# Optimization experiments

Hardware: AMD Instinct MI355X
Metric: run time of the kernel (lower is better)

## Reference

```python
import jax, jax.numpy as jnp
import numpy as np
from jax import lax


def grid_sample(img, grid):
    """Bilinear grid_sample, align_corners=True, zeros padding.
    img: [N, C, H, W]; grid: [N, Hg, Wg, 2] with (x, y) in [-1, 1].
    Returns [N, C, Hg, Wg]."""
    N, C, H, W = img.shape
    Hg, Wg = grid.shape[1], grid.shape[2]
    gx = (grid[..., 0] + 1.0) * 0.5 * (W - 1)
    gy = (grid[..., 1] + 1.0) * 0.5 * (H - 1)
    x0 = jnp.floor(gx); y0 = jnp.floor(gy)
    x1 = x0 + 1.0;      y1 = y0 + 1.0
    wx1 = gx - x0; wx0 = 1.0 - wx1
    wy1 = gy - y0; wy0 = 1.0 - wy1
    flat = img.reshape(N, C, H * W)

    def corner(ix, iy, w):
        valid = (ix >= 0) & (ix <= W - 1) & (iy >= 0) & (iy <= H - 1)
        ixc = jnp.clip(ix, 0, W - 1).astype(jnp.int32)
        iyc = jnp.clip(iy, 0, H - 1).astype(jnp.int32)
        idx = (iyc * W + ixc).reshape(N, -1)                      # [N, Hg*Wg]
        vals = jnp.take_along_axis(flat, idx[:, None, :], axis=2)  # [N, C, Hg*Wg]
        return vals * (w * valid).reshape(N, 1, -1)

    out = (corner(x0, y0, wx0 * wy0) + corner(x1, y0, wx1 * wy0)
           + corner(x0, y1, wx0 * wy1) + corner(x1, y1, wx1 * wy1))
    return out.reshape(N, C, Hg, Wg)


def ref_points(H, W, dtype=jnp.float32):
    # normalized reference points in (y, x) order, align with torch linspace(0.5, H-0.5, H)
    ry = ((jnp.arange(H, dtype=dtype) + 0.5) / H) * 2.0 - 1.0
    rx = ((jnp.arange(W, dtype=dtype) + 0.5) / W) * 2.0 - 1.0
    gy, gx = jnp.meshgrid(ry, rx, indexing='ij')
    return jnp.stack([gy, gx], axis=-1)  # [H, W, 2]


def conv1x1(x, w, b=None):
    # x: [B, Cin, H, W], w: [Cout, Cin]
    y = jnp.einsum('bchw,oc->bohw', x, w)
    if b is not None:
        y = y + b[None, :, None, None]
    return y


def setup_inputs() -> dict:
    key = jax.random.key(0)
    ks = jax.random.split(key, 16)
    B, nc, H, W = 4, 512, 32, 32
    heads, hc = 8, 64
    gc = 512  # n_group_channels (n_groups = 1)
    s = lambda fan: 1.0 / np.sqrt(fan)
    inp = {
        'x': jax.random.normal(ks[0], (B, nc, H, W), jnp.float32),
        'dw_w': jax.random.normal(ks[1], (gc, 1, 3, 3), jnp.float32) * s(9),
        'dw_b': jnp.zeros((gc,), jnp.float32),
        'ln_w': jnp.ones((gc,), jnp.float32),
        'ln_b': jnp.zeros((gc,), jnp.float32),
        'pw_w': jax.random.normal(ks[2], (2, gc), jnp.float32) * s(gc),
        'q_w': jax.random.normal(ks[3], (nc, nc), jnp.float32) * s(nc),
        'q_b': jnp.zeros((nc,), jnp.float32),
        'k_w': jax.random.normal(ks[4], (nc, nc), jnp.float32) * s(nc),
        'k_b': jnp.zeros((nc,), jnp.float32),
        'v_w': jax.random.normal(ks[5], (nc, nc), jnp.float32) * s(nc),
        'v_b': jnp.zeros((nc,), jnp.float32),
        'rpe_table': jax.random.normal(ks[6], (heads, 2 * H - 1, 2 * W - 1), jnp.float32) * 0.01,
        'gamma': jnp.full((1,), 0.1, jnp.float32),
    }
    return inp


def reference(x, dw_w, dw_b, ln_w, ln_b, pw_w, q_w, q_b, k_w, k_b, v_w, v_b, rpe_table, gamma):
    B, C, H, W = x.shape
    heads, hc = 8, 64
    g = 1
    gc = C // g
    gh = heads // g
    scale = hc ** (-0.5)
    offset_range_factor = 2.0

    # q projection (1x1 conv)
    q = conv1x1(x, q_w, q_b)                                       # [B, C, H, W]

    # offset network: depthwise 3x3 conv -> channel LayerNorm -> GELU -> 1x1 conv to 2ch
    q_off = q.reshape(B * g, gc, H, W)
    h = lax.conv_general_dilated(q_off, dw_w, (1, 1), 'SAME',
                                 dimension_numbers=('NCHW', 'OIHW', 'NCHW'),
                                 feature_group_count=gc)
    h = h + dw_b[None, :, None, None]
    mu = jnp.mean(h, axis=1, keepdims=True)
    var = jnp.mean(jnp.square(h - mu), axis=1, keepdims=True)
    h = (h - mu) * lax.rsqrt(var + 1e-5)
    h = h * ln_w[None, :, None, None] + ln_b[None, :, None, None]
    h = jax.nn.gelu(h, approximate=False)
    offset = jnp.einsum('bchw,oc->bohw', h, pw_w)                  # [B*g, 2, Hk, Wk]
    Hk, Wk = offset.shape[2], offset.shape[3]
    n = Hk * Wk
    rng = jnp.array([1.0 / Hk, 1.0 / Wk], x.dtype).reshape(1, 2, 1, 1)
    offset = jnp.tanh(offset) * rng * offset_range_factor
    offset = jnp.transpose(offset, (0, 2, 3, 1))                   # [B*g, Hk, Wk, 2] (y, x)

    reference_pts = ref_points(Hk, Wk, x.dtype)                    # [Hk, Wk, 2]
    pos = offset + reference_pts[None]                             # [B*g, Hk, Wk, 2]

    # deformable feature sampling
    x_sampled = grid_sample(x.reshape(B * g, gc, H, W), pos[..., ::-1])
    x_sampled = x_sampled.reshape(B, C, n)                         # [B, C, n]

    k = jnp.einsum('oc,bcn->bon', k_w, x_sampled) + k_b[None, :, None]
    v = jnp.einsum('oc,bcn->bon', v_w, x_sampled) + v_b[None, :, None]

    qf = q.reshape(B, heads, hc, H * W)
    kf = k.reshape(B, heads, hc, n)
    vf = v.reshape(B, heads, hc, n)

    attn = jnp.einsum('bhcm,bhcn->bhmn', qf, kf) * scale           # [B, heads, HW, n]

    # relative position bias via grid_sample over rpe table
    rpe = jnp.broadcast_to(rpe_table[None], (B, heads, 2 * H - 1, 2 * W - 1))
    rpe = rpe.reshape(B * g, gh, 2 * H - 1, 2 * W - 1)
    q_grid = ref_points(H, W, x.dtype).reshape(H * W, 2)           # [HW, 2]
    disp = (q_grid[None, :, None, :] - pos.reshape(B * g, n, 2)[:, None, :, :]) * 0.5
    bias = grid_sample(rpe, disp[..., ::-1])                       # [B*g, gh, HW, n]
    attn = attn + bias.reshape(B, heads, H * W, n)

    attn = jax.nn.softmax(attn, axis=-1)
    out = jnp.einsum('bhmn,bhcn->bhcm', attn, vf).reshape(B, C, H, W)
    out = gamma.reshape(()) * out + x
    return out, attn.reshape(B * heads, H * W, n)
```

## Files before the change

kernel.cpp:

```cpp
#include <hip/hip_runtime.h>
#include <hip/hip_bf16.h>
#include <math.h>

typedef short bf16x8 __attribute__((ext_vector_type(8)));
typedef _Float16 f16x8 __attribute__((ext_vector_type(8)));
typedef float f32x4 __attribute__((ext_vector_type(4)));
typedef _Float16 h2 __attribute__((ext_vector_type(2)));

__device__ inline short f2bf(float f) {
    union { float f; unsigned u; } v; v.f = f;
    unsigned r = v.u + 0x7FFFu + ((v.u >> 16) & 1u);
    return (short)(r >> 16);
}
__device__ inline float bf2f(short s) {
    union { unsigned u; float f; } v; v.u = ((unsigned)(unsigned short)s) << 16;
    return v.f;
}
__device__ inline h2 pkrtz(float a, float b) {
    return __builtin_bit_cast(h2, __builtin_amdgcn_cvt_pkrtz(a, b));
}
__device__ inline float fast_exp2(float x) {
    float r;
    asm("v_exp_f32 %0, %1" : "=v"(r) : "v"(x));
    return r;
}
__device__ inline float dot2(h2 a, h2 b) {
#if __has_builtin(__builtin_amdgcn_fdot2)
    return __builtin_amdgcn_fdot2(a, b, 0.f, false);
#else
    return (float)a[0] * (float)b[0] + (float)a[1] * (float)b[1];
#endif
}
__device__ inline void nt_store4(float4 v, float* p) {
    __builtin_nontemporal_store(__builtin_bit_cast(f32x4, v), (f32x4*)p);
}

__global__ __launch_bounds__(256) void prep_x(
    const float* __restrict__ x, short* __restrict__ xt,
    const float* __restrict__ qw, const float* __restrict__ kw,
    const float* __restrict__ vw, short* __restrict__ qwb,
    short* __restrict__ kwb, short* __restrict__ vwb,
    const float* __restrict__ rpe, unsigned* __restrict__ rpet)
{
    __shared__ float ts[64][65];
    int t = threadIdx.x;
    if (blockIdx.z == 5) {
        if (blockIdx.y != 0 || blockIdx.x >= 8) return;
        int hh = blockIdx.x;
        const float* rh = rpe + hh * 3969;
        const float L2E = 1.44269504f;
        #pragma unroll
        for (int i = 0; i < 17; ++i) {
            int j = i * 256 + t;
            if (j < 4225) {
                int iy = j / 65;
                int ix = j - iy * 65;
                float v0 = 0.f, v1 = 0.f;
                if (iy >= 1 && iy <= 63) {
                    const float* rr = rh + (iy - 1) * 63;
                    if (ix >= 1 && ix <= 63) v0 = rr[ix - 1] * L2E;
                    if (ix <= 62)            v1 = rr[ix] * L2E;
                }
                h2 pr; pr[0] = (_Float16)v0; pr[1] = (_Float16)v1;
                rpet[hh * 4225 + j] = __builtin_bit_cast(unsigned, pr);
            }
        }
        return;
    }
    if (blockIdx.z == 4) {
        int f = blockIdx.y * 16 + blockIdx.x;
        int base = (f * 256 + t) * 8;
        #pragma unroll
        for (int w = 0; w < 3; ++w) {
            const float* src = (w == 0) ? qw : (w == 1) ? kw : vw;
            short* dst = (w == 0) ? qwb : (w == 1) ? kwb : vwb;
            float4 f0 = *(const float4*)(src + base);
            float4 f1 = *(const float4*)(src + base + 4);
            bf16x8 o;
            o[0] = f2bf(f0.x); o[1] = f2bf(f0.y); o[2] = f2bf(f0.z); o[3] = f2bf(f0.w);
            o[4] = f2bf(f1.x); o[5] = f2bf(f1.y); o[6] = f2bf(f1.z); o[7] = f2bf(f1.w);
            *(bf16x8*)(dst + base) = o;
        }
        return;
    }
    int p0 = blockIdx.x * 64, c0 = blockIdx.y * 64, b = blockIdx.z;
    #pragma unroll
    for (int i = 0; i < 16; ++i) {
        int idx = i * 256 + t;
        int cl = idx >> 6, pl = idx & 63;
        ts[cl][pl] = x[((size_t)(b * 512 + c0 + cl)) * 1024 + p0 + pl];
    }
    __syncthreads();
    #pragma unroll
    for (int i = 0; i < 16; ++i) {
        int idx = i * 256 + t;
        int pl = idx >> 6, cl = idx & 63;
        xt[((size_t)(b * 1024 + p0 + pl)) * 512 + c0 + cl] = f2bf(ts[cl][pl]);
    }
}

__device__ inline void nt_tile_64x128(const short* __restrict__ A,
                                      const short* __restrict__ B,
                                      int m0, int n0, int t,
                                      short (*As)[32], short (*Bs)[32],
                                      f32x4 (&acc)[2][4])
{
    int wid = t >> 6, l = t & 63;
    int wm = wid >> 1, wn = wid & 1;
    int srB = t >> 1, halfB = t & 1;
    int swB = (srB >> 1) & 3;
    int sB0 = (halfB * 2) ^ swB, sB1 = (halfB * 2 + 1) ^ swB;
    int srA = t >> 2, qA = t & 3;
    int sA = qA ^ ((srA >> 1) & 3);
    for (int k0 = 0; k0 < 512; k0 += 32) {
        const int4 a0 = *(const int4*)(A + (size_t)(m0 + srA) * 512 + k0 + qA * 8);
        const int4 b0 = *(const int4*)(B + (size_t)(n0 + srB) * 512 + k0 + halfB * 16);
        const int4 b1 = *(const int4*)(B + (size_t)(n0 + srB) * 512 + k0 + halfB * 16 + 8);
        __syncthreads();
        *(int4*)&As[srA][sA * 8] = a0;
        *(int4*)&Bs[srB][sB0 * 8] = b0;
        *(int4*)&Bs[srB][sB1 * 8] = b1;
        __syncthreads();
        bf16x8 af[2], bfr[4];
        #pragma unroll
        for (int mt = 0; mt < 2; ++mt) {
            int r = wm * 32 + mt * 16 + (l & 15);
            af[mt] = *(const bf16x8*)&As[r][(((l >> 4)) ^ ((r >> 1) & 3)) * 8];
        }
        #pragma unroll
        for (int nt = 0; nt < 4; ++nt) {
            int r = wn * 64 + nt * 16 + (l & 15);
            bfr[nt] = *(const bf16x8*)&Bs[r][(((l >> 4)) ^ ((r >> 1) & 3)) * 8];
        }
        #pragma unroll
        for (int mt = 0; mt < 2; ++mt)
            #pragma unroll
            for (int nt = 0; nt < 4; ++nt)
                acc[mt][nt] = __builtin_amdgcn_mfma_f32_16x16x32_bf16(
                    af[mt], bfr[nt], acc[mt][nt], 0, 0, 0);
    }
}

__global__ __launch_bounds__(256) void gemm_q(
    const short* __restrict__ A, const short* __restrict__ B,
    const float* __restrict__ bias, short* __restrict__ Ob)
{
    __shared__ short As[64][32];
    __shared__ short Bs[128][32];
    int m0 = blockIdx.x * 64, n0 = blockIdx.y * 128;
    int t = threadIdx.x, wid = t >> 6, l = t & 63;
    int wm = wid >> 1, wn = wid & 1;
    f32x4 acc[2][4] = {};
    nt_tile_64x128(A, B, m0, n0, t, As, Bs, acc);
    #pragma unroll
    for (int mt = 0; mt < 2; ++mt)
        #pragma unroll
        for (int nt = 0; nt < 4; ++nt)
            #pragma unroll
            for (int r = 0; r < 4; ++r) {
                int m = m0 + wm * 32 + mt * 16 + (l >> 4) * 4 + r;
                int n = n0 + wn * 64 + nt * 16 + (l & 15);
                Ob[(size_t)m * 512 + n] = f2bf(acc[mt][nt][r] + bias[n]);
            }
}

__global__ __launch_bounds__(256) void gemm_kv(
    const short* __restrict__ xsb, const short* __restrict__ kwb,
    const float* __restrict__ k_b, short* __restrict__ kfr,
    const short* __restrict__ vwb, const float* __restrict__ v_b,
    short* __restrict__ vfr)
{
    __shared__ short As[64][32];
    __shared__ short Bs[128][32];
    int bid = blockIdx.x;
    int t = threadIdx.x, wid = t >> 6, l = t & 63;
    int wm = wid >> 1, wn = wid & 1;
    f32x4 acc[2][4] = {};
    if (bid < 256) {
        int m0 = (bid >> 5) * 64, n0 = (bid & 31) * 128;
        nt_tile_64x128(kwb, xsb, m0, n0, t, As, Bs, acc);
        int h = m0 >> 6;
        #pragma unroll
        for (int mt = 0; mt < 2; ++mt) {
            int ch0 = m0 + wm * 32 + mt * 16 + (l >> 4) * 4;
            float4 kb4 = *(const float4*)(k_b + ch0);
            int frag = (ch0 >> 5) & 1, gg = (ch0 >> 3) & 3, e = ch0 & 7;
            #pragma unroll
            for (int nt = 0; nt < 4; ++nt) {
                int sm = n0 + wn * 64 + nt * 16 + (l & 15);
                int bq = sm >> 10, p = sm & 1023;
                int T = p >> 4, cs = p & 15;
                uint2 w;
                w.x = (unsigned)(unsigned short)f2bf(acc[mt][nt][0] + kb4.x)
                    | ((unsigned)(unsigned short)f2bf(acc[mt][nt][1] + kb4.y) << 16);
                w.y = (unsigned)(unsigned short)f2bf(acc[mt][nt][2] + kb4.z)
                    | ((unsigned)(unsigned short)f2bf(acc[mt][nt][3] + kb4.w) << 16);
                *(uint2*)(kfr + ((((size_t)(bq * 8 + h) * 64 + T) * 2 + frag) * 64
                                 + gg * 16 + cs) * 8 + e) = w;
            }
        }
    } else {
        int id2 = bid - 256;
        int z = id2 >> 6, rr2 = id2 & 63;
        int m0 = (rr2 >> 2) * 64, n0 = (rr2 & 3) * 128;
        nt_tile_64x128(xsb + (size_t)z * 524288, vwb, m0, n0, t, As, Bs, acc);
        #pragma unroll
        for (int mt = 0; mt < 2; ++mt) {
            int p0 = m0 + wm * 32 + mt * 16 + (l >> 4) * 4;
            int cc = p0 >> 5, gg = (p0 >> 3) & 3, e = p0 & 7;
            #pragma unroll
            for (int nt = 0; nt < 4; ++nt) {
                int ch = n0 + wn * 64 + nt * 16 + (l & 15);
                int h = ch >> 6, wg = (ch & 63) >> 4, cs = ch & 15;
                float vb = v_b[ch];
                h2 plo, phi;
                plo[0] = (_Float16)(acc[mt][nt][0] + vb);
                plo[1] = (_Float16)(acc[mt][nt][1] + vb);
                phi[0] = (_Float16)(acc[mt][nt][2] + vb);
                phi[1] = (_Float16)(acc[mt][nt][3] + vb);
                uint2 w;
                w.x = __builtin_bit_cast(unsigned, plo);
                w.y = __builtin_bit_cast(unsigned, phi);
                *(uint2*)(vfr + ((((size_t)(z * 8 + h) * 4 + wg) * 32 + cc) * 64
                                 + gg * 16 + cs) * 8 + e) = w;
            }
        }
    }
}

__global__ __launch_bounds__(256) void offset_sample(
    const short* __restrict__ qbf, const float* __restrict__ dw_w,
    const float* __restrict__ dw_b, const float* __restrict__ ln_w,
    const float* __restrict__ ln_b, const float* __restrict__ pw_w,
    const short* __restrict__ xt, float* __restrict__ pos,
    short* __restrict__ xs)
{
    __shared__ float red[8];
    __shared__ float2 psh;
    int bid = blockIdx.x;
    int b = bid >> 10, p = bid & 1023;
    int y = p >> 5, x = p & 31;
    int t = threadIdx.x;
    int c0 = 2 * t;
    const short* qb = qbf + (size_t)b * 524288;
    float h0, h1;
    {
        const float* w0 = dw_w + c0 * 9;
        const float* w1 = w0 + 9;
        float s0 = 0.f, s1 = 0.f;
        #pragma unroll
        for (int ky = 0; ky < 3; ++ky) {
            int yy = y + ky - 1;
            if (yy < 0 || yy > 31) continue;
            #pragma unroll
            for (int kx = 0; kx < 3; ++kx) {
                int xx = x + kx - 1;
                if (xx < 0 || xx > 31) continue;
                unsigned u = *(const unsigned*)(qb + (size_t)(yy * 32 + xx) * 512 + c0);
                s0 += bf2f((short)(u & 0xFFFF)) * w0[ky * 3 + kx];
                s1 += bf2f((short)(u >> 16)) * w1[ky * 3 + kx];
            }
        }
        float2 db = *(const float2*)(dw_b + c0);
        h0 = s0 + db.x; h1 = s1 + db.y;
    }
    float ls = h0 + h1;
    float lq = h0 * h0 + h1 * h1;
    #pragma unroll
    for (int s = 32; s >= 1; s >>= 1) {
        ls += __shfl_xor(ls, s);
        lq += __shfl_xor(lq, s);
    }
    int wid = t >> 6, lane = t & 63;
    if (lane == 0) { red[wid] = ls; red[4 + wid] = lq; }
    __syncthreads();
    float mu  = (red[0] + red[1] + red[2] + red[3]) * (1.f / 512.f);
    float var = (red[4] + red[5] + red[6] + red[7]) * (1.f / 512.f) - mu * mu;
    float rstd = rsqrtf(var + 1e-5f);
    float o0, o1;
    {
        float2 lw = *(const float2*)(ln_w + c0);
        float2 lb = *(const float2*)(ln_b + c0);
        float2 p0 = *(const float2*)(pw_w + c0);
        float2 p1 = *(const float2*)(pw_w + 512 + c0);
        float hn0 = (h0 - mu) * rstd * lw.x + lb.x;
        float hn1 = (h1 - mu) * rstd * lw.y + lb.y;
        float g0 = 0.5f * hn0 * (1.f + erff(hn0 * 0.70710678118f));
        float g1 = 0.5f * hn1 * (1.f + erff(hn1 * 0.70710678118f));
        o0 = g0 * p0.x + g1 * p0.y;
        o1 = g0 * p1.x + g1 * p1.y;
    }
    #pragma unroll
    for (int s = 32; s >= 1; s >>= 1) {
        o0 += __shfl_xor(o0, s);
        o1 += __shfl_xor(o1, s);
    }
    __syncthreads();
    if (lane == 0) { red[wid] = o0; red[4 + wid] = o1; }
    __syncthreads();
    if (t == 0) {
        float oy = tanhf(red[0] + red[1] + red[2] + red[3]) * 0.0625f;
        float ox = tanhf(red[4] + red[5] + red[6] + red[7]) * 0.0625f;
        float ry = ((y + 0.5f) * (1.f / 32.f)) * 2.f - 1.f;
        float rx = ((x + 0.5f) * (1.f / 32.f)) * 2.f - 1.f;
        float py = oy + ry, px = ox + rx;
        pos[bid * 2]     = py;
        pos[bid * 2 + 1] = px;
        psh = make_float2(py, px);
    }
    __syncthreads();
    float py = psh.x, px = psh.y;
    float gx = (px + 1.f) * 15.5f;
    float gy = (py + 1.f) * 15.5f;
    float x0f = floorf(gx), y0f = floorf(gy);
    int ix0 = (int)x0f, iy0 = (int)y0f;
    float wx1 = gx - x0f, wx0 = 1.f - wx1;
    float wy1 = gy - y0f, wy0 = 1.f - wy1;
    const short* base = xt + (size_t)b * 524288;
    float a0 = 0.f, a1 = 0.f;
    #pragma unroll
    for (int tap = 0; tap < 4; ++tap) {
        int ix = ix0 + (tap & 1), iy = iy0 + (tap >> 1);
        float w = ((tap & 1) ? wx1 : wx0) * ((tap >> 1) ? wy1 : wy0);
        if (ix >= 0 && ix < 32 && iy >= 0 && iy < 32) {
            unsigned u = *(const unsigned*)(base + (size_t)(iy * 32 + ix) * 512 + c0);
            a0 += bf2f((short)(u & 0xFFFF)) * w;
            a1 += bf2f((short)(u >> 16)) * w;
        }
    }
    unsigned o = ((unsigned)(unsigned short)f2bf(a0)) |
                 (((unsigned)(unsigned short)f2bf(a1)) << 16);
    *(unsigned*)(xs + (size_t)bid * 512 + c0) = o;
}

__global__ __launch_bounds__(512, 4) void attn_fused(
    const short* __restrict__ qbf, const short* __restrict__ kfr,
    const short* __restrict__ vfr, const float* __restrict__ pos,
    const unsigned* __restrict__ rpet, const float* __restrict__ x,
    const float* __restrict__ gamma, float* __restrict__ attn_out,
    float* __restrict__ out0)
{
    __shared__ __align__(16) char smem_raw[33024];
    __shared__ float S_part[16][8];
    h2*     rpe_s = (h2*)smem_raw;
    float2* ccs   = (float2*)(smem_raw + 16960);
    short*  Pn    = (short*)smem_raw;

    int bid = blockIdx.x;
    int xcd = bid & 7, seq = bid >> 3;
    int m0 = (seq & 63) * 16;
    int bh = xcd + 8 * (seq >> 6);
    int b = bh >> 3, h = bh & 7;
    int t = threadIdx.x, wn = t >> 6, l = t & 63;
    int g = l >> 4, c16 = l & 15;

    const unsigned* rt = rpet + h * 4225;
    #pragma unroll
    for (int i = 0; i < 9; ++i) {
        int e = i * 512 + t;
        if (e < 4225) ((unsigned*)rpe_s)[e] = rt[e];
    }
    #pragma unroll
    for (int i = 0; i < 2; ++i) {
        int idx = i * 512 + t;
        float2 pf = *(const float2*)(pos + b * 2048 + idx * 2);
        ccs[idx] = make_float2(fmaf(-15.5f, pf.x, 32.f), fmaf(-15.5f, pf.y, 32.f));
    }
    int rowm = m0 + c16;
    const short* qrow = qbf + ((size_t)(b * 1024 + rowm) * 512 + h * 64 + g * 8);
    bf16x8 aq0 = *(const bf16x8*)qrow;
    bf16x8 aq1 = *(const bf16x8*)(qrow + 32);
    float qy = (((rowm >> 5) + 0.5f) * (1.f / 16.f) - 1.f) * 15.5f;
    float qx = (((rowm & 31) + 0.5f) * (1.f / 16.f) - 1.f) * 15.5f;
    __syncthreads();

    float Ssum = 0.f;
    float e0, e1;
    unsigned ep[16];
    const short* kr = kfr + (size_t)(bh * 64 + wn * 8) * 1024 + l * 8;
    bf16x8 ka0 = *(const bf16x8*)kr;
    bf16x8 kb0 = *(const bf16x8*)(kr + 512);
    bf16x8 ka1 = *(const bf16x8*)(kr + 1024);
    bf16x8 kb1 = *(const bf16x8*)(kr + 1536);
    #pragma unroll
    for (int nt = 0; nt < 8; ++nt) {
        bf16x8 bk0 = ka0, bk1 = kb0;
        ka0 = ka1; kb0 = kb1;
        if (nt < 6) {
            ka1 = *(const bf16x8*)(kr + (nt + 2) * 1024);
            kb1 = *(const bf16x8*)(kr + (nt + 2) * 1024 + 512);
        }
        __builtin_amdgcn_s_setprio(1);
        f32x4 acc = {0.f, 0.f, 0.f, 0.f};
        acc = __builtin_amdgcn_mfma_f32_16x16x32_bf16(bk0, aq0, acc, 0, 0, 0);
        acc = __builtin_amdgcn_mfma_f32_16x16x32_bf16(bk1, aq1, acc, 0, 0, 0);
        __builtin_amdgcn_s_setprio(0);
        int nb = wn * 128 + nt * 16;
        #pragma unroll
        for (int r = 0; r < 4; ++r) {
            float2 cc = ccs[nb + g * 4 + r];
            float gyp = qy + cc.x;
            float gxp = qx + cc.y;
            float fy = floorf(gyp), fx = floorf(gxp);
            float wy1 = gyp - fy, wx1 = gxp - fx;
            int ad = (int)(fy * 65.f + fx);
            h2 r0 = rpe_s[ad];
            h2 r1 = rpe_s[ad + 65];
            h2 wp = pkrtz(1.f - wx1, wx1);
            float t0 = dot2(r0, wp);
            float t1 = dot2(r1, wp);
            float bias2 = t0 + wy1 * (t1 - t0);
            float logit2 = fmaf(acc[r], 0.1803368801f, bias2);
            float e = fast_exp2(logit2);
            Ssum += e;
            if (r == 0) e0 = e;
            else if (r == 1) ep[nt * 2] = __builtin_bit_cast(unsigned, pkrtz(e0, e));
            else if (r == 2) e1 = e;
            else ep[nt * 2 + 1] = __builtin_bit_cast(unsigned, pkrtz(e1, e));
        }
    }
    Ssum += __shfl_xor(Ssum, 16);
    Ssum += __shfl_xor(Ssum, 32);
    if (l < 16) S_part[c16][wn] = Ssum;
    __syncthreads();
    float4 sa = *(const float4*)&S_part[c16][0];
    float4 sb = *(const float4*)&S_part[c16][4];
    float invS = 1.f / (sa.x + sa.y + sa.z + sa.w + sb.x + sb.y + sb.z + sb.w);

    short* prow = Pn + c16 * 1032 + wn * 128;
    #pragma unroll
    for (int nt = 0; nt < 8; ++nt) {
        uint2 w;
        w.x = ep[nt * 2];
        w.y = ep[nt * 2 + 1];
        *(uint2*)(prow + nt * 16 + g * 4) = w;
    }
    __syncthreads();

    size_t obase = ((size_t)(bh * 1024 + m0)) * 1024;
    if (wn >= 4) {
        int tw = t - 256;
        #pragma unroll
        for (int row = 0; row < 16; ++row) {
            float ivr = __shfl(invS, row);
            const unsigned* pr = (const unsigned*)(Pn + row * 1032 + tw * 4);
            unsigned u0 = pr[0], u1 = pr[1];
            h2 a = __builtin_bit_cast(h2, u0);
            h2 bb = __builtin_bit_cast(h2, u1);
            float4 vv = make_float4((float)a[0] * ivr, (float)a[1] * ivr,
                                    (float)bb[0] * ivr, (float)bb[1] * ivr);
            nt_store4(vv, attn_out + obase + (size_t)row * 1024 + tw * 4);
        }
    } else {
        const short* Vb = vfr + (size_t)((bh * 4 + wn) * 32) * 512;
        const short* Prow = Pn + c16 * 1032 + g * 8;
        f32x4 dacc = {0.f, 0.f, 0.f, 0.f};
        __builtin_amdgcn_s_setprio(1);
        #pragma unroll
        for (int cc = 0; cc < 32; ++cc) {
            f16x8 pa  = *(const f16x8*)(Prow + cc * 32);
            f16x8 vb8 = *(const f16x8*)(Vb + cc * 512 + l * 8);
            dacc = __builtin_amdgcn_mfma_f32_16x16x32_f16(pa, vb8, dacc, 0, 0, 0);
        }
        __builtin_amdgcn_s_setprio(0);
        float gm = gamma[0];
        float gi0 = gm * __shfl(invS, g * 4);
        float gi1 = gm * __shfl(invS, g * 4 + 1);
        float gi2 = gm * __shfl(invS, g * 4 + 2);
        float gi3 = gm * __shfl(invS, g * 4 + 3);
        int ch = h * 64 + wn * 16 + c16;
        int m = m0 + g * 4;
        size_t idx = ((size_t)(b * 512 + ch)) * 1024 + m;
        float4 xv = *(const float4*)(x + idx);
        float4 ov;
        ov.x = gi0 * dacc[0] + xv.x;
        ov.y = gi1 * dacc[1] + xv.y;
        ov.z = gi2 * dacc[2] + xv.z;
        ov.w = gi3 * dacc[3] + xv.w;
        nt_store4(ov, out0 + idx);
    }
}

extern "C" void kernel_launch(void* const* d_in, const int* in_sizes, int n_in,
                              void* d_out, int out_size, void* d_ws, size_t ws_size,
                              hipStream_t stream) {
    const float* x     = (const float*)d_in[0];
    const float* dw_w  = (const float*)d_in[1];
    const float* dw_b  = (const float*)d_in[2];
    const float* ln_w  = (const float*)d_in[3];
    const float* ln_b  = (const float*)d_in[4];
    const float* pw_w  = (const float*)d_in[5];
    const float* q_w   = (const float*)d_in[6];
    const float* q_b   = (const float*)d_in[7];
    const float* k_w   = (const float*)d_in[8];
    const float* k_b   = (const float*)d_in[9];
    const float* v_w   = (const float*)d_in[10];
    const float* v_b   = (const float*)d_in[11];
    const float* rpe   = (const float*)d_in[12];
    const float* gamma = (const float*)d_in[13];

    float* out0 = (float*)d_out;
    float* attn = out0 + (size_t)4 * 512 * 1024;

    char* w = (char*)d_ws;
    short*    xt   = (short*)w;
    short*    qwb  = (short*)(w + 4194304);
    short*    kwb  = (short*)(w + 4718592);
    short*    vwb  = (short*)(w + 5242880);
    short*    qbf  = (short*)(w + 5767168);
    short*    xsb  = (short*)(w + 9961472);
    short*    kfr  = (short*)(w + 14155776);
    short*    vfr  = (short*)(w + 18350080);
    float*    pos  = (float*)(w + 22544384);
    unsigned* rpet = (unsigned*)(w + 22577152);

    prep_x<<<dim3(16, 8, 6), 256, 0, stream>>>(x, xt, q_w, k_w, v_w, qwb, kwb,
                                               vwb, rpe, rpet);
    gemm_q<<<dim3(64, 4), 256, 0, stream>>>(xt, qwb, q_b, qbf);
    offset_sample<<<4096, 256, 0, stream>>>(qbf, dw_w, dw_b, ln_w, ln_b, pw_w,
                                            xt, pos, xsb);
    gemm_kv<<<512, 256, 0, stream>>>(xsb, kwb, k_b, kfr, vwb, v_b, vfr);
    attn_fused<<<2048, 512, 0, stream>>>(qbf, kfr, vfr, pos, rpet, x,
                                         gamma, attn, out0);
}
```

Baseline: 109.2 us.

## Pack RPE bilinear quad into uint2 table and merge softmax sum barrier

```diff
diff --git a/kernel.cpp b/kernel.cpp
--- a/kernel.cpp
+++ b/kernel.cpp
@@ -40,7 +40,7 @@
     const float* __restrict__ qw, const float* __restrict__ kw,
     const float* __restrict__ vw, short* __restrict__ qwb,
     short* __restrict__ kwb, short* __restrict__ vwb,
-    const float* __restrict__ rpe, unsigned* __restrict__ rpet)
+    const float* __restrict__ rpe, uint2* __restrict__ rpet)
 {
     __shared__ float ts[64][65];
     int t = threadIdx.x;
@@ -49,21 +49,21 @@
         int hh = blockIdx.x;
         const float* rh = rpe + hh * 3969;
         const float L2E = 1.44269504f;
-        #pragma unroll
-        for (int i = 0; i < 17; ++i) {
+        auto P = [&](int y, int xx) -> float {
+            return (y >= 1 && y <= 63 && xx >= 1 && xx <= 63)
+                 ? rh[(y - 1) * 63 + (xx - 1)] * L2E : 0.f;
+        };
+        #pragma unroll
+        for (int i = 0; i < 16; ++i) {
             int j = i * 256 + t;
-            if (j < 4225) {
-                int iy = j / 65;
-                int ix = j - iy * 65;
-                float v0 = 0.f, v1 = 0.f;
-                if (iy >= 1 && iy <= 63) {
-                    const float* rr = rh + (iy - 1) * 63;
-                    if (ix >= 1 && ix <= 63) v0 = rr[ix - 1] * L2E;
-                    if (ix <= 62)            v1 = rr[ix] * L2E;
-                }
-                h2 pr; pr[0] = (_Float16)v0; pr[1] = (_Float16)v1;
-                rpet[hh * 4225 + j] = __builtin_bit_cast(unsigned, pr);
-            }
+            int qy = j >> 6, qx = j & 63;
+            h2 lo, hi;
+            lo[0] = (_Float16)P(qy, qx);     lo[1] = (_Float16)P(qy, qx + 1);
+            hi[0] = (_Float16)P(qy + 1, qx); hi[1] = (_Float16)P(qy + 1, qx + 1);
+            uint2 w;
+            w.x = __builtin_bit_cast(unsigned, lo);
+            w.y = __builtin_bit_cast(unsigned, hi);
+            rpet[hh * 4096 + j] = w;
         }
         return;
     }
@@ -336,15 +336,15 @@
 __global__ __launch_bounds__(512, 4) void attn_fused(
     const short* __restrict__ qbf, const short* __restrict__ kfr,
     const short* __restrict__ vfr, const float* __restrict__ pos,
-    const unsigned* __restrict__ rpet, const float* __restrict__ x,
+    const uint2* __restrict__ rpet, const float* __restrict__ x,
     const float* __restrict__ gamma, float* __restrict__ attn_out,
     float* __restrict__ out0)
 {
-    __shared__ __align__(16) char smem_raw[33024];
-    __shared__ float S_part[16][8];
-    h2*     rpe_s = (h2*)smem_raw;
-    float2* ccs   = (float2*)(smem_raw + 16960);
-    short*  Pn    = (short*)smem_raw;
+    __shared__ __align__(16) char smem_raw[40960];
+    uint2*  rpq    = (uint2*)smem_raw;
+    float*  ccsf   = (float*)(smem_raw + 32768);
+    short*  Pn     = (short*)smem_raw;
+    float*  S_part = (float*)(smem_raw + 33536);
 
     int bid = blockIdx.x;
     int xcd = bid & 7, seq = bid >> 3;
@@ -354,17 +354,16 @@
     int t = threadIdx.x, wn = t >> 6, l = t & 63;
     int g = l >> 4, c16 = l & 15;
 
-    const unsigned* rt = rpet + h * 4225;
-    #pragma unroll
-    for (int i = 0; i < 9; ++i) {
-        int e = i * 512 + t;
-        if (e < 4225) ((unsigned*)rpe_s)[e] = rt[e];
-    }
+    const uint2* rt = rpet + h * 4096;
+    #pragma unroll
+    for (int i = 0; i < 8; ++i)
+        rpq[i * 512 + t] = rt[i * 512 + t];
     #pragma unroll
     for (int i = 0; i < 2; ++i) {
         int idx = i * 512 + t;
         float2 pf = *(const float2*)(pos + b * 2048 + idx * 2);
-        ccs[idx] = make_float2(fmaf(-15.5f, pf.x, 32.f), fmaf(-15.5f, pf.y, 32.f));
+        ccsf[idx * 2]     = fmaf(-15.5f, pf.x, 32.f);
+        ccsf[idx * 2 + 1] = fmaf(-15.5f, pf.y, 32.f);
     }
     int rowm = m0 + c16;
     const short* qrow = qbf + ((size_t)(b * 1024 + rowm) * 512 + h * 64 + g * 8);
@@ -396,19 +395,24 @@
         acc = __builtin_amdgcn_mfma_f32_16x16x32_bf16(bk1, aq1, acc, 0, 0, 0);
         __builtin_amdgcn_s_setprio(0);
         int nb = wn * 128 + nt * 16;
+        const float* cbase = ccsf + (nb + g * 4) * 2;
+        float4 c01 = *(const float4*)cbase;
+        float4 c23 = *(const float4*)(cbase + 4);
         #pragma unroll
         for (int r = 0; r < 4; ++r) {
-            float2 cc = ccs[nb + g * 4 + r];
-            float gyp = qy + cc.x;
-            float gxp = qx + cc.y;
+            float cy = (r == 0) ? c01.x : (r == 1) ? c01.z : (r == 2) ? c23.x : c23.z;
+            float cx = (r == 0) ? c01.y : (r == 1) ? c01.w : (r == 2) ? c23.y : c23.w;
+            float gyp = qy + cy;
+            float gxp = qx + cx;
             float fy = floorf(gyp), fx = floorf(gxp);
             float wy1 = gyp - fy, wx1 = gxp - fx;
-            int ad = (int)(fy * 65.f + fx);
-            h2 r0 = rpe_s[ad];
-            h2 r1 = rpe_s[ad + 65];
+            int ad = (int)(fy * 64.f + fx);
+            uint2 q4 = rpq[ad];
+            h2 lo = __builtin_bit_cast(h2, q4.x);
+            h2 hi = __builtin_bit_cast(h2, q4.y);
             h2 wp = pkrtz(1.f - wx1, wx1);
-            float t0 = dot2(r0, wp);
-            float t1 = dot2(r1, wp);
+            float t0 = dot2(lo, wp);
+            float t1 = dot2(hi, wp);
             float bias2 = t0 + wy1 * (t1 - t0);
             float logit2 = fmaf(acc[r], 0.1803368801f, bias2);
             float e = fast_exp2(logit2);
@@ -421,12 +425,8 @@
     }
     Ssum += __shfl_xor(Ssum, 16);
     Ssum += __shfl_xor(Ssum, 32);
-    if (l < 16) S_part[c16][wn] = Ssum;
-    __syncthreads();
-    float4 sa = *(const float4*)&S_part[c16][0];
-    float4 sb = *(const float4*)&S_part[c16][4];
-    float invS = 1.f / (sa.x + sa.y + sa.z + sa.w + sb.x + sb.y + sb.z + sb.w);
-
+    __syncthreads();
+    if (l < 16) S_part[c16 * 8 + wn] = Ssum;
     short* prow = Pn + c16 * 1032 + wn * 128;
     #pragma unroll
     for (int nt = 0; nt < 8; ++nt) {
@@ -436,6 +436,9 @@
         *(uint2*)(prow + nt * 16 + g * 4) = w;
     }
     __syncthreads();
+    float4 sa = *(const float4*)&S_part[c16 * 8];
+    float4 sb = *(const float4*)&S_part[c16 * 8 + 4];
+    float invS = 1.f / (sa.x + sa.y + sa.z + sa.w + sb.x + sb.y + sb.z + sb.w);
 
     size_t obase = ((size_t)(bh * 1024 + m0)) * 1024;
     if (wn >= 4) {
@@ -443,10 +446,9 @@
         #pragma unroll
         for (int row = 0; row < 16; ++row) {
             float ivr = __shfl(invS, row);
-            const unsigned* pr = (const unsigned*)(Pn + row * 1032 + tw * 4);
-            unsigned u0 = pr[0], u1 = pr[1];
-            h2 a = __builtin_bit_cast(h2, u0);
-            h2 bb = __builtin_bit_cast(h2, u1);
+            uint2 pr8 = *(const uint2*)(Pn + row * 1032 + tw * 4);
+            h2 a = __builtin_bit_cast(h2, pr8.x);
+            h2 bb = __builtin_bit_cast(h2, pr8.y);
             float4 vv = make_float4((float)a[0] * ivr, (float)a[1] * ivr,
                                     (float)bb[0] * ivr, (float)bb[1] * ivr);
             nt_store4(vv, attn_out + obase + (size_t)row * 1024 + tw * 4);
@@ -512,7 +514,7 @@
     short*    kfr  = (short*)(w + 14155776);
     short*    vfr  = (short*)(w + 18350080);
     float*    pos  = (float*)(w + 22544384);
-    unsigned* rpet = (unsigned*)(w + 22577152);
+    uint2*    rpet = (uint2*)(w + 22577152);
 
     prep_x<<<dim3(16, 8, 6), 256, 0, stream>>>(x, xt, q_w, k_w, v_w, qwb, kwb,
                                                vwb, rpe, rpet);
```

Result: no change. 108.9 us (-0.3%).
